# Performance work log

Measured on AMD Instinct MI355X. Metric: run time of the kernel, lower is better.

Reference implementation:

```python
import jax, jax.numpy as jnp
import numpy as np
import itertools

SEQ, NF, K, SD, NB, NC, NOBJ = 8, 4, 3, 256, 512, 174, 10
BELTA, SUB, BATCH = 0.1, 10, 256
SCALES = list(range(NF, 0, -1))  # [4, 3, 2, 1]
D = (K + 1) * SD                 # per-frame fused feature dim = 1024


def _adjust_scales(seq_ind, is_test):
    # mirrors adjust_scale_train / adjust_scale_test
    scale_max = NF * 2
    if seq_ind < scale_max:
        return SCALES[-seq_ind:] if is_test else SCALES[-min(SUB, seq_ind):]
    return SCALES[:min(SUB, seq_ind) + 1]


def _plan(is_test):
    # Static (non-traced) relation-index plan: for each seq_ind, the set of
    # arithmetic-progression frame combinations selected by select_idx().
    plan = []
    for seq_ind in range(1, SEQ + 1):
        entries = []
        for scale in _adjust_scales(seq_ind, is_test):
            k = min(scale, seq_ind)
            division = seq_ind // scale
            sel = [r for r in itertools.combinations(range(seq_ind), k)
                   if np.all(np.diff(np.asarray(r)) == division)]
            if sel:
                entries.append((scale, np.asarray(sel, dtype=np.int32)))
        plan.append(entries)
    return plan


def _temporal_variation(init_input):
    # VLAD-style soft residuals. Source runs kmeans (non-deterministic,
    # numpy/detached); we use deterministic centers = first K points per clip
    # and reproduce the exact downstream math, including the (buggy but
    # faithful) scalar spectral-norm soft assignment shared by all points.
    x = init_input.reshape(-1, SEQ, NOBJ, SD)              # (B, S, O, d)
    flat = x.reshape(x.shape[0], SEQ * NOBJ, SD)           # (B, N, d)
    centers = flat[:, :K, :]                               # (B, K, d)
    diff = flat[:, None, :, :] - centers[:, :, None, :]    # (B, K, N, d)
    sig = jnp.linalg.svd(diff, compute_uv=False)[..., 0]   # matrix 2-norm per (b, k)
    w = jax.nn.softmax(-BELTA * sig ** 2, axis=-1)         # (B, K), same for every point
    # S[b,t,k,:] = sum_o w[b,k] * (x[b,t,o,:] - c[b,k,:])
    var = w[:, None, :, None] * (x.sum(axis=2)[:, :, None, :] - NOBJ * centers[:, None, :, :])
    return jax.lax.stop_gradient(var)  # source detaches via .detach().numpy()


def _fusion(x, w1, b1, w2, b2):
    # Sequential(ReLU, Linear, ReLU, Linear)
    h = jnp.maximum(jax.nn.relu(x) @ w1 + b1, 0.0)
    return h @ w2 + b2


def _forward(graph_out, init_input, params, is_test):
    B = graph_out.shape[0]
    var = _temporal_variation(init_input)                      # (B, S, K, d)
    new_input = jnp.concatenate([var.reshape(B, SEQ, K * SD), graph_out], axis=2)  # (B, S, D)
    rows = []
    for entries in _plan(bool(is_test)):
        acc = jnp.zeros((B, NC), graph_out.dtype)
        for scale, rel in entries:
            # batched gather of all sampled relations at once: (B, R, scale, D)
            g = new_input[:, rel, :].reshape(B, rel.shape[0], scale * D)
            acc = acc + _fusion(g, *params[scale]).sum(axis=1)
        rows.append(acc)
    return jnp.stack(rows, axis=1).reshape(B * SEQ, NC)


def setup_inputs():
    key = jax.random.key(0)
    ks = jax.random.split(key, 2 + 2 * len(SCALES))
    inp = {
        "graph_out": jax.random.normal(ks[0], (BATCH, SEQ, SD), jnp.float32),
        "init_input": jax.random.normal(ks[1], (BATCH * SEQ, NOBJ, SD), jnp.float32),
        "is_test": 0,
    }
    for i, s in enumerate(SCALES):
        inp[f"w1_{s}"] = jax.random.normal(ks[2 + 2 * i], (s * D, NB), jnp.float32) * 0.02
        inp[f"b1_{s}"] = jnp.zeros((NB,), jnp.float32)
        inp[f"w2_{s}"] = jax.random.normal(ks[3 + 2 * i], (NB, NC), jnp.float32) * 0.02
        inp[f"b2_{s}"] = jnp.zeros((NC,), jnp.float32)
    return inp


def reference(graph_out, init_input, is_test, w1_4, b1_4, w2_4, b2_4, w1_3, b1_3, w2_3, b2_3, w1_2, b1_2, w2_2, b2_2, w1_1, b1_1, w2_1, b2_1):
    params = {4: (w1_4, b1_4, w2_4, b2_4), 3: (w1_3, b1_3, w2_3, b2_3),
              2: (w1_2, b1_2, w2_2, b2_2), 1: (w1_1, b1_1, w2_1, b2_1)}
    return _forward(graph_out, init_input, params, is_test)
```

## Files before the change

### kernel.cpp

```cpp
#include <hip/hip_runtime.h>
#include <math.h>
#include <stdint.h>


typedef __attribute__((ext_vector_type(8))) short short8v;
typedef __attribute__((ext_vector_type(4))) short short4v;
typedef __attribute__((ext_vector_type(4))) float f32x4;

__device__ __forceinline__ short f2bf(float f) {
  uint32_t u = __float_as_uint(f);
  u += 0x7fffu + ((u >> 16) & 1u);
  return (short)(u >> 16);
}
__device__ __forceinline__ float bf2f(short s) {
  return __uint_as_float(((uint32_t)(uint16_t)s) << 16);
}
__device__ __forceinline__ void gload16(const void* g, void* l) {
  __builtin_amdgcn_global_load_lds(
      (const __attribute__((address_space(1))) void*)g,
      (__attribute__((address_space(3))) void*)l, 16, 0, 0);
}

__device__ const int8_t ROWS4[12][5] = {
  {3, 0,1,2,3},
  {4, 0,1,2,3},{4, 1,2,3,4},
  {5, 0,1,2,3},{5, 1,2,3,4},{5, 2,3,4,5},
  {6, 0,1,2,3},{6, 1,2,3,4},{6, 2,3,4,5},{6, 3,4,5,6},
  {7, 0,2,4,6},{7, 1,3,5,7},
};
__device__ const int8_t ROWS3[15][4] = {
  {2, 0,1,2},
  {3, 0,1,2},{3, 1,2,3},
  {4, 0,1,2},{4, 1,2,3},{4, 2,3,4},
  {5, 0,2,4},{5, 1,3,5},
  {6, 0,2,4},{6, 1,3,5},{6, 2,4,6},
  {7, 0,2,4},{7, 1,3,5},{7, 2,4,6},{7, 3,5,7},
};
__device__ const int8_t ROWS2[19][3] = {
  {1, 0,1},
  {2, 0,1},{2, 1,2},
  {3, 0,2},{3, 1,3},
  {4, 0,2},{4, 1,3},{4, 2,4},
  {5, 0,3},{5, 1,4},{5, 2,5},
  {6, 0,3},{6, 1,4},{6, 2,5},{6, 3,6},
  {7, 0,4},{7, 1,5},{7, 2,6},{7, 3,7},
};
__device__ const int8_t ROWS1[36][2] = {
  {0,0},
  {1,0},{1,1},
  {2,0},{2,1},{2,2},
  {3,0},{3,1},{3,2},{3,3},
  {4,0},{4,1},{4,2},{4,3},{4,4},
  {5,0},{5,1},{5,2},{5,3},{5,4},{5,5},
  {6,0},{6,1},{6,2},{6,3},{6,4},{6,5},{6,6},
  {7,0},{7,1},{7,2},{7,3},{7,4},{7,5},{7,6},{7,7},
};
__device__ const float CNT[8][4] = {
  {0,0,0,1},{0,0,1,2},{0,1,2,3},{1,2,2,4},
  {2,3,3,5},{3,2,3,6},{4,3,4,7},{2,4,4,8},
};

#define GV_FH    0
#define GV_FL    20480
#define GV_S     40960
#define GV_XSUM  67840
#define GV_VB    76032
#define GV_UU    78048
#define GV_SCAL  79008
#define GV_SZ    79056

__global__ __launch_bounds__(256) void gram_var(
    const float* __restrict__ init, const float* __restrict__ graph,
    short* __restrict__ Rbuf)
{
  __shared__ __align__(16) char smem[GV_SZ];
  short* Fh  = (short*)(smem + GV_FH);
  short* Fl  = (short*)(smem + GV_FL);
  float* Sm  = (float*)(smem + GV_S);
  float* xsm = (float*)(smem + GV_XSUM);
  float* vb  = (float*)(smem + GV_VB);
  float* uum = (float*)(smem + GV_UU);
  float* scal= (float*)(smem + GV_SCAL);

  const int tid = threadIdx.x, lane = tid & 63, w = tid >> 6;
  const int b = blockIdx.x;
  const float* fb = init + (size_t)b * 80 * 256;

  int ti_[7], tj_[7];
#pragma unroll
  for (int q = 0; q < 7; ++q) {
    int tt = w + q * 4;
    int t5 = (tt < 25) ? tt : 0;
    ti_[q] = t5 / 5; tj_[q] = t5 % 5;
  }

  f32x4 acc[7];
#pragma unroll
  for (int q = 0; q < 7; ++q) acc[q] = (f32x4){0.f, 0.f, 0.f, 0.f};

  for (int ch = 0; ch < 2; ++ch) {
    __syncthreads();
    {
      const int t = tid >> 5, kq = tid & 31;
      const float* src = fb + (size_t)(t * 10) * 256 + ch * 128 + kq * 4;
      f32x4 sum = (f32x4){0.f, 0.f, 0.f, 0.f};
#pragma unroll
      for (int o = 0; o < 10; ++o) {
        f32x4 v = *(const f32x4*)(src + (size_t)o * 256);
        int r = t * 10 + o;
        int byte8 = r * 256 + ((kq * 8) ^ ((r & 7) << 4));
        short4v hv, lv;
#pragma unroll
        for (int e = 0; e < 4; ++e) {
          short h = f2bf(v[e]);
          hv[e] = h;
          lv[e] = f2bf(v[e] - bf2f(h));
        }
        *(short4v*)((char*)Fh + byte8) = hv;
        *(short4v*)((char*)Fl + byte8) = lv;
        sum += v;
      }
      *(f32x4*)(xsm + t * 256 + ch * 128 + kq * 4) = sum;
    }
    __syncthreads();

#pragma unroll
    for (int ks = 0; ks < 4; ++ks) {
      const int koff2 = (ks * 32 + (lane >> 4) * 8) * 2;
#pragma unroll
      for (int q = 0; q < 7; ++q) {
        const int tt = w + q * 4;
        if (tt < 25) {
          int ra = ti_[q] * 16 + (lane & 15);
          int rb = tj_[q] * 16 + (lane & 15);
          int ba = ra * 256 + (koff2 ^ ((ra & 7) << 4));
          int bb = rb * 256 + (koff2 ^ ((rb & 7) << 4));
          short8v ah = *(const short8v*)((char*)Fh + ba);
          short8v al = *(const short8v*)((char*)Fl + ba);
          short8v bh = *(const short8v*)((char*)Fh + bb);
          short8v bl = *(const short8v*)((char*)Fl + bb);
          acc[q] = __builtin_amdgcn_mfma_f32_16x16x32_bf16(ah, bh, acc[q], 0, 0, 0);
          acc[q] = __builtin_amdgcn_mfma_f32_16x16x32_bf16(ah, bl, acc[q], 0, 0, 0);
          acc[q] = __builtin_amdgcn_mfma_f32_16x16x32_bf16(al, bh, acc[q], 0, 0, 0);
        }
      }
    }
  }

#pragma unroll
  for (int q = 0; q < 7; ++q) {
    const int tt = w + q * 4;
    if (tt < 25) {
      int row0 = ti_[q] * 16 + (lane >> 4) * 4;
      int col = tj_[q] * 16 + (lane & 15);
#pragma unroll
      for (int r = 0; r < 4; ++r) Sm[(row0 + r) * 84 + col] = acc[q][r];
    }
  }
  if (tid < 240) vb[(0 * 3 + tid / 80) * 84 + (tid % 80)] = 1.0f;
  __syncthreads();

  const int pk = (tid < 240) ? tid / 80 : 0;
  const int pi = (tid < 240) ? tid % 80 : 0;
  int cur = 0;
  for (int it = 0; it < 5; ++it) {
    const bool last = (it == 4);
    float u = 0.f;
    if (tid < 240) {
      const float* Si = Sm + pi * 84;
      const float* vk = vb + (cur * 3 + pk) * 84;
#pragma unroll
      for (int q2 = 0; q2 < 20; ++q2) {
        f32x4 aa = *(const f32x4*)(Si + q2 * 4);
        f32x4 vv = *(const f32x4*)(vk + q2 * 4);
        u += aa.x * vv.x + aa.y * vv.y + aa.z * vv.z + aa.w * vv.w;
      }
    } else if (tid < 246) {
      int w2 = tid - 240;
      int k = (w2 < 3) ? w2 : w2 - 3;
      const float* vk = vb + (cur * 3 + k) * 84;
      float s = 0.f;
      if (w2 < 3) {
        for (int j2 = 0; j2 < 80; ++j2) s += vk[j2];
        scal[k] = s;
      } else {
        const float* Sk = Sm + k * 84;
        for (int j2 = 0; j2 < 80; ++j2) s += Sk[j2] * vk[j2];
        scal[3 + k] = s;
      }
    }
    __syncthreads();
    if (tid < 240) {
      float sg = scal[pk], tu = scal[3 + pk];
      float un = u - Sm[pi * 84 + pk] * sg - tu + Sm[pk * 84 + pk] * sg;
      if (!last) vb[((cur ^ 1) * 3 + pk) * 84 + pi] = un * 6.103515625e-05f;
      else       uum[pk * 80 + pi] = un;
    }
    __syncthreads();
    if (!last) cur ^= 1;
  }

  if (tid < 192) {
    const int k = tid >> 6, ln = tid & 63;
    float v1 = vb[(cur * 3 + k) * 84 + ln];
    float u1 = uum[k * 80 + ln];
    float a = u1 * v1, b2 = v1 * v1;
    if (ln < 16) {
      float v2 = vb[(cur * 3 + k) * 84 + 64 + ln];
      float u2 = uum[k * 80 + 64 + ln];
      a += u2 * v2; b2 += v2 * v2;
    }
#pragma unroll
    for (int m = 32; m >= 1; m >>= 1) {
      a += __shfl_xor(a, m);
      b2 += __shfl_xor(b2, m);
    }
    if (ln == 0) scal[9 + k] = a / b2;
  }
  __syncthreads();
  if (tid == 0) {
    float L0 = -0.1f * scal[9], L1 = -0.1f * scal[10], L2 = -0.1f * scal[11];
    float m = fmaxf(L0, fmaxf(L1, L2));
    float e0 = expf(L0 - m), e1 = expf(L1 - m), e2 = expf(L2 - m);
    float inv = 1.0f / (e0 + e1 + e2);
    scal[6] = e0 * inv; scal[7] = e1 * inv; scal[8] = e2 * inv;
  }
  __syncthreads();

  {
    const float w0 = scal[6], w1 = scal[7], w2 = scal[8];
    const int d0 = (tid & 63) * 4;
#pragma unroll
    for (int p = 0; p < 2; ++p) {
      const int t = p * 4 + (tid >> 6);
      f32x4 xs = *(const f32x4*)(xsm + t * 256 + d0);
      f32x4 c0 = *(const f32x4*)(fb + 0 * 256 + d0);
      f32x4 c1 = *(const f32x4*)(fb + 1 * 256 + d0);
      f32x4 c2 = *(const f32x4*)(fb + 2 * 256 + d0);
      f32x4 go = *(const f32x4*)(graph + (size_t)(b * 8 + t) * 256 + d0);
      size_t rb = ((size_t)(b * 8 + t)) * 1024;
      short4v s0, s1, s2, s3;
#pragma unroll
      for (int q = 0; q < 4; ++q) {
        float xq = xs[q];
        s0[q] = f2bf(fmaxf(w0 * (xq - 10.f * c0[q]), 0.f));
        s1[q] = f2bf(fmaxf(w1 * (xq - 10.f * c1[q]), 0.f));
        s2[q] = f2bf(fmaxf(w2 * (xq - 10.f * c2[q]), 0.f));
        s3[q] = f2bf(fmaxf(go[q], 0.f));
      }
      *(short4v*)&Rbuf[rb + 0 + d0]   = s0;
      *(short4v*)&Rbuf[rb + 256 + d0] = s1;
      *(short4v*)&Rbuf[rb + 512 + d0] = s2;
      *(short4v*)&Rbuf[rb + 768 + d0] = s3;
    }
  }
}

__global__ __launch_bounds__(512) void prep_weights(
    const float* __restrict__ w1_4, const float* __restrict__ w1_3,
    const float* __restrict__ w1_2, const float* __restrict__ w1_1,
    const float* __restrict__ w2a, const float* __restrict__ w2b,
    const float* __restrict__ w2c, const float* __restrict__ w2d,
    short* __restrict__ W1T, short* __restrict__ W2T)
{
  __shared__ float sh[64 * 65];
  const int blk = blockIdx.x, tid = threadIdx.x;
  if (blk < 1280) {
    const int slice = blk >> 7, rem = blk & 127;
    const int k0 = (rem & 15) * 64, c0 = (rem >> 4) * 64;
    const float* W1; int j;
    if (slice < 4)      { W1 = w1_4; j = slice; }
    else if (slice < 7) { W1 = w1_3; j = slice - 4; }
    else if (slice < 9) { W1 = w1_2; j = slice - 7; }
    else                { W1 = w1_1; j = 0; }
#pragma unroll
    for (int q = tid; q < 1024; q += 512) {
      int r = q >> 4, cq = (q & 15) * 4;
      f32x4 v = *(const f32x4*)(W1 + (size_t)(j * 1024 + k0 + r) * 512 + c0 + cq);
      sh[r * 65 + cq + 0] = v.x; sh[r * 65 + cq + 1] = v.y;
      sh[r * 65 + cq + 2] = v.z; sh[r * 65 + cq + 3] = v.w;
    }
    __syncthreads();
#pragma unroll
    for (int q = tid; q < 1024; q += 512) {
      int cc = q >> 4, kq = (q & 15) * 4;
      short4v sv;
#pragma unroll
      for (int m = 0; m < 4; ++m) sv[m] = f2bf(sh[(kq + m) * 65 + cc]);
      *(short4v*)&W1T[(size_t)(slice * 512 + c0 + cc) * 1024 + k0 + kq] = sv;
    }
  } else {
    int idx = (blk - 1280) * 2048 + tid * 4;
    int col = idx >> 11, kg = idx & 2047;
    int si = kg >> 9, kr = kg & 511;
    const float* w = (si == 0) ? w2a : (si == 1) ? w2b : (si == 2) ? w2c : w2d;
    short4v sv;
#pragma unroll
    for (int q = 0; q < 4; ++q)
      sv[q] = (col < 174) ? f2bf(w[(size_t)(kr + q) * 174 + col]) : (short)0;
    *(short4v*)&W2T[idx] = sv;
  }
}

__global__ __launch_bounds__(256) void p_mfma(
    const short* __restrict__ A, const short* __restrict__ W1T,
    short* __restrict__ P)
{
  __shared__ short As[128 * 32];
  __shared__ short Bs[128 * 32];
  const int id = blockIdx.x + blockIdx.y * 40;
  const int nid = (id & 7) * 80 + (id >> 3);
  const int bx = nid >> 4, by = nid & 15;
  const int tid = threadIdx.x, lane = tid & 63, w = tid >> 6;
  const int wr = w >> 1, wc = w & 1;
  const int rowBase = by * 128;
  const short* Bp = W1T + (size_t)bx * 128 * 1024;
  const int rA = w * 16 + (lane >> 2);
  const int kkA = (lane & 3) * 8;

  f32x4 acc[4][4];
#pragma unroll
  for (int m = 0; m < 4; ++m)
#pragma unroll
    for (int n = 0; n < 4; ++n) acc[m][n] = (f32x4){0.f, 0.f, 0.f, 0.f};

  for (int k0 = 0; k0 < 1024; k0 += 32) {
    __syncthreads();
    gload16(A + (size_t)(rowBase + rA) * 1024 + k0 + kkA, As + w * 512);
    gload16(A + (size_t)(rowBase + 64 + rA) * 1024 + k0 + kkA, As + 2048 + w * 512);
    gload16(Bp + (size_t)rA * 1024 + k0 + kkA, Bs + w * 512);
    gload16(Bp + (size_t)(64 + rA) * 1024 + k0 + kkA, Bs + 2048 + w * 512);
    __syncthreads();
    short8v a[4], bv[4];
#pragma unroll
    for (int m = 0; m < 4; ++m)
      a[m] = *(const short8v*)(As + (wr * 64 + m * 16 + (lane & 15)) * 32 + (lane >> 4) * 8);
#pragma unroll
    for (int n = 0; n < 4; ++n)
      bv[n] = *(const short8v*)(Bs + (wc * 64 + n * 16 + (lane & 15)) * 32 + (lane >> 4) * 8);
#pragma unroll
    for (int m = 0; m < 4; ++m)
#pragma unroll
      for (int n = 0; n < 4; ++n)
        acc[m][n] = __builtin_amdgcn_mfma_f32_16x16x32_bf16(a[m], bv[n], acc[m][n], 0, 0, 0);
  }

  const int colG = bx * 128 + wc * 64;
#pragma unroll
  for (int m = 0; m < 4; ++m) {
    int row = rowBase + wr * 64 + m * 16 + (lane >> 4) * 4;
#pragma unroll
    for (int n = 0; n < 4; ++n) {
      int col = colG + n * 16 + (lane & 15);
#pragma unroll
      for (int r = 0; r < 4; ++r)
        P[(size_t)(row + r) * 5120 + col] = f2bf(acc[m][n][r]);
    }
  }
}

__global__ __launch_bounds__(256) void hsum_all(
    const short* __restrict__ P,
    const float* __restrict__ b1a, const float* __restrict__ b1b,
    const float* __restrict__ b1c, const float* __restrict__ b1d,
    short* __restrict__ Hsum)
{
  const int row = blockIdx.x, t = row & 7, base = row - t;
  const int c0 = threadIdx.x * 2;
  const size_t prow = (size_t)base * 5120;

  {
    float2 bb = *(const float2*)(b1a + c0);
    float a0 = 0.f, a1 = 0.f;
    for (int r = 0; r < 12; ++r) {
      if (ROWS4[r][0] != t) continue;
      float h0 = bb.x, h1 = bb.y;
#pragma unroll
      for (int jj = 0; jj < 4; ++jj) {
        const short2 pv = *(const short2*)(P + prow + (size_t)ROWS4[r][1 + jj] * 5120 + jj * 512 + c0);
        h0 += bf2f(pv.x); h1 += bf2f(pv.y);
      }
      a0 += fmaxf(h0, 0.f); a1 += fmaxf(h1, 0.f);
    }
    uint32_t wv = (uint32_t)(uint16_t)f2bf(a0) | ((uint32_t)(uint16_t)f2bf(a1) << 16);
    *(uint32_t*)&Hsum[(size_t)row * 2048 + c0] = wv;
  }
  {
    float2 bb = *(const float2*)(b1b + c0);
    float a0 = 0.f, a1 = 0.f;
    for (int r = 0; r < 15; ++r) {
      if (ROWS3[r][0] != t) continue;
      float h0 = bb.x, h1 = bb.y;
#pragma unroll
      for (int jj = 0; jj < 3; ++jj) {
        const short2 pv = *(const short2*)(P + prow + (size_t)ROWS3[r][1 + jj] * 5120 + 2048 + jj * 512 + c0);
        h0 += bf2f(pv.x); h1 += bf2f(pv.y);
      }
      a0 += fmaxf(h0, 0.f); a1 += fmaxf(h1, 0.f);
    }
    uint32_t wv = (uint32_t)(uint16_t)f2bf(a0) | ((uint32_t)(uint16_t)f2bf(a1) << 16);
    *(uint32_t*)&Hsum[(size_t)row * 2048 + 512 + c0] = wv;
  }
  {
    float2 bb = *(const float2*)(b1c + c0);
    float a0 = 0.f, a1 = 0.f;
    for (int r = 0; r < 19; ++r) {
      if (ROWS2[r][0] != t) continue;
      float h0 = bb.x, h1 = bb.y;
#pragma unroll
      for (int jj = 0; jj < 2; ++jj) {
        const short2 pv = *(const short2*)(P + prow + (size_t)ROWS2[r][1 + jj] * 5120 + 3584 + jj * 512 + c0);
        h0 += bf2f(pv.x); h1 += bf2f(pv.y);
      }
      a0 += fmaxf(h0, 0.f); a1 += fmaxf(h1, 0.f);
    }
    uint32_t wv = (uint32_t)(uint16_t)f2bf(a0) | ((uint32_t)(uint16_t)f2bf(a1) << 16);
    *(uint32_t*)&Hsum[(size_t)row * 2048 + 1024 + c0] = wv;
  }
  {
    float2 bb = *(const float2*)(b1d + c0);
    float a0 = 0.f, a1 = 0.f;
    for (int r = 0; r < 36; ++r) {
      if (ROWS1[r][0] != t) continue;
      const short2 pv = *(const short2*)(P + prow + (size_t)ROWS1[r][1] * 5120 + 4608 + c0);
      a0 += fmaxf(bb.x + bf2f(pv.x), 0.f);
      a1 += fmaxf(bb.y + bf2f(pv.y), 0.f);
    }
    uint32_t wv = (uint32_t)(uint16_t)f2bf(a0) | ((uint32_t)(uint16_t)f2bf(a1) << 16);
    *(uint32_t*)&Hsum[(size_t)row * 2048 + 1536 + c0] = wv;
  }
}

__global__ __launch_bounds__(256) void out_split(
    const short* __restrict__ H, const short* __restrict__ W2T,
    float* __restrict__ partial)
{
  __shared__ short As[128 * 32];
  __shared__ short Bs[64 * 32];
  const int tid = threadIdx.x, lane = tid & 63, w = tid >> 6;
  const int wr = w >> 1, wc = w & 1;
  const int rowBase = blockIdx.y * 128, colBase = blockIdx.x * 64;
  const int kBase = blockIdx.z * 512;
  const int rA = w * 16 + (lane >> 2);
  const int kkA = (lane & 3) * 8;

  f32x4 acc[4][2];
#pragma unroll
  for (int m = 0; m < 4; ++m)
#pragma unroll
    for (int n = 0; n < 2; ++n) acc[m][n] = (f32x4){0.f, 0.f, 0.f, 0.f};

  for (int k0 = 0; k0 < 512; k0 += 32) {
    const int kg = kBase + k0;
    __syncthreads();
    gload16(H + (size_t)(rowBase + rA) * 2048 + kg + kkA, As + w * 512);
    gload16(H + (size_t)(rowBase + 64 + rA) * 2048 + kg + kkA, As + 2048 + w * 512);
    gload16(W2T + (size_t)(colBase + rA) * 2048 + kg + kkA, Bs + w * 512);
    __syncthreads();
    short8v a[4], bv[2];
#pragma unroll
    for (int m = 0; m < 4; ++m)
      a[m] = *(const short8v*)(As + (wr * 64 + m * 16 + (lane & 15)) * 32 + (lane >> 4) * 8);
#pragma unroll
    for (int n = 0; n < 2; ++n)
      bv[n] = *(const short8v*)(Bs + (wc * 32 + n * 16 + (lane & 15)) * 32 + (lane >> 4) * 8);
#pragma unroll
    for (int m = 0; m < 4; ++m)
#pragma unroll
      for (int n = 0; n < 2; ++n)
        acc[m][n] = __builtin_amdgcn_mfma_f32_16x16x32_bf16(a[m], bv[n], acc[m][n], 0, 0, 0);
  }

  float* pz = partial + (size_t)blockIdx.z * 2048 * 192;
#pragma unroll
  for (int n = 0; n < 2; ++n) {
    int col = colBase + wc * 32 + n * 16 + (lane & 15);
#pragma unroll
    for (int m = 0; m < 4; ++m) {
      int row0 = rowBase + wr * 64 + m * 16 + (lane >> 4) * 4;
#pragma unroll
      for (int r = 0; r < 4; ++r)
        pz[(size_t)(row0 + r) * 192 + col] = acc[m][n][r];
    }
  }
}

__global__ __launch_bounds__(256) void out_reduce(
    const float* __restrict__ partial,
    const float* __restrict__ b2a, const float* __restrict__ b2b,
    const float* __restrict__ b2c, const float* __restrict__ b2d,
    float* __restrict__ out)
{
  const int row = blockIdx.x, col = threadIdx.x;
  if (col >= 174) return;
  const size_t o = (size_t)row * 192 + col;
  float s = partial[o] + partial[o + (size_t)2048 * 192]
          + partial[o + (size_t)4096 * 192] + partial[o + (size_t)6144 * 192];
  int tt = row & 7;
  float bias = CNT[tt][0] * b2a[col] + CNT[tt][1] * b2b[col]
             + CNT[tt][2] * b2c[col] + CNT[tt][3] * b2d[col];
  out[(size_t)row * 174 + col] = s + bias;
}

extern "C" void kernel_launch(void* const* d_in, const int* in_sizes, int n_in,
                              void* d_out, int out_size, void* d_ws, size_t ws_size,
                              hipStream_t stream) {
  const float* graph = (const float*)d_in[0];
  const float* init  = (const float*)d_in[1];
  const float* w1[4] = {(const float*)d_in[3],  (const float*)d_in[7],
                        (const float*)d_in[11], (const float*)d_in[15]};
  const float* b1[4] = {(const float*)d_in[4],  (const float*)d_in[8],
                        (const float*)d_in[12], (const float*)d_in[16]};
  const float* w2[4] = {(const float*)d_in[5],  (const float*)d_in[9],
                        (const float*)d_in[13], (const float*)d_in[17]};
  const float* b2[4] = {(const float*)d_in[6],  (const float*)d_in[10],
                        (const float*)d_in[14], (const float*)d_in[18]};
  float* out = (float*)d_out;

  char* ws = (char*)d_ws;
  short* Rbf  = (short*)(ws + 0);
  short* W1T  = (short*)(ws + ((size_t)4  << 20));
  short* P    = (short*)(ws + ((size_t)14 << 20));
  short* W2T  = (short*)(ws + ((size_t)34 << 20));
  short* Hsum = (short*)(ws + 0);
  float* Part = (float*)(ws + ((size_t)8 << 20));

  gram_var<<<256, 256, 0, stream>>>(init, graph, Rbf);

  prep_weights<<<1472, 512, 0, stream>>>(w1[0], w1[1], w1[2], w1[3],
                                         w2[0], w2[1], w2[2], w2[3], W1T, W2T);

  p_mfma<<<dim3(40, 16), 256, 0, stream>>>(Rbf, W1T, P);

  hsum_all<<<2048, 256, 0, stream>>>(P, b1[0], b1[1], b1[2], b1[3], Hsum);

  out_split<<<dim3(3, 16, 4), 256, 0, stream>>>(Hsum, W2T, Part);

  out_reduce<<<2048, 256, 0, stream>>>(Part, b2[0], b2[1], b2[2], b2[3], out);
}
```

Baseline: 94.45 us.

## Compute only needed frame-slot projections in P GEMM and vectorize hsum

The projection GEMM previously computed all 10 weight-slice columns for every frame row, although each slice is only consumed for a contiguous subset of frame positions. It now enumerates (slice, row-tile, col-tile) work items and gathers only the frame rows each slice actually uses, storing P in a compact per-slice layout. The GEMM blocks drop from 640 to 408, with matching reductions in P write traffic. hsum_all is updated to index the compact layout and now processes two rows per block with 4-wide vector loads. This adds per-row div/mod index math and a gathered A-load pattern.

```diff
diff --git a/kernel.cpp b/kernel.cpp
--- a/kernel.cpp
+++ b/kernel.cpp
@@ -60,6 +60,11 @@
   {2,3,3,5},{3,2,3,6},{4,3,4,7},{2,4,4,8},
 };
 
+__device__ const int SL_LO[10]  = {0,1,2,3, 0,1,2, 0,1, 0};
+__device__ const int SL_LEN[10] = {4,4,4,5, 4,5,6, 4,7, 8};
+__device__ const int SL_PB[10]  = {0,4,8,12,17,21,26,32,36,43};
+__device__ const int SL_MT[10]  = {0,8,16,24,34,42,52,64,72,86};
+
 #define GV_FH    0
 #define GV_FL    20480
 #define GV_S     40960
@@ -308,15 +313,26 @@
 {
   __shared__ short As[128 * 32];
   __shared__ short Bs[128 * 32];
-  const int id = blockIdx.x + blockIdx.y * 40;
-  const int nid = (id & 7) * 80 + (id >> 3);
-  const int bx = nid >> 4, by = nid & 15;
+  const int id = blockIdx.x;
+  const int nid = (id & 7) * 51 + (id >> 3);
+  const int ctile = nid & 3;
+  const int rest = nid >> 2;
+  int sl = 0;
+#pragma unroll
+  for (int q = 1; q < 10; ++q) if (rest >= SL_MT[q]) sl = q;
+  const int mt = rest - SL_MT[sl];
+  const int lo = SL_LO[sl];
+  const unsigned len = (unsigned)SL_LEN[sl];
+  short* Pp = P + (size_t)SL_PB[sl] * 131072;
+  const short* Bp = W1T + ((size_t)sl * 512 + (size_t)ctile * 128) * 1024;
+
   const int tid = threadIdx.x, lane = tid & 63, w = tid >> 6;
   const int wr = w >> 1, wc = w & 1;
-  const int rowBase = by * 128;
-  const short* Bp = W1T + (size_t)bx * 128 * 1024;
   const int rA = w * 16 + (lane >> 2);
   const int kkA = (lane & 3) * 8;
+  const unsigned lr0 = (unsigned)(mt * 128 + rA), lr1 = lr0 + 64u;
+  const int gr0 = (int)((lr0 / len) * 8u + lo + (lr0 % len));
+  const int gr1 = (int)((lr1 / len) * 8u + lo + (lr1 % len));
 
   f32x4 acc[4][4];
 #pragma unroll
@@ -326,8 +342,8 @@
 
   for (int k0 = 0; k0 < 1024; k0 += 32) {
     __syncthreads();
-    gload16(A + (size_t)(rowBase + rA) * 1024 + k0 + kkA, As + w * 512);
-    gload16(A + (size_t)(rowBase + 64 + rA) * 1024 + k0 + kkA, As + 2048 + w * 512);
+    gload16(A + (size_t)gr0 * 1024 + k0 + kkA, As + w * 512);
+    gload16(A + (size_t)gr1 * 1024 + k0 + kkA, As + 2048 + w * 512);
     gload16(Bp + (size_t)rA * 1024 + k0 + kkA, Bs + w * 512);
     gload16(Bp + (size_t)(64 + rA) * 1024 + k0 + kkA, Bs + 2048 + w * 512);
     __syncthreads();
@@ -345,16 +361,15 @@
         acc[m][n] = __builtin_amdgcn_mfma_f32_16x16x32_bf16(a[m], bv[n], acc[m][n], 0, 0, 0);
   }
 
-  const int colG = bx * 128 + wc * 64;
 #pragma unroll
   for (int m = 0; m < 4; ++m) {
-    int row = rowBase + wr * 64 + m * 16 + (lane >> 4) * 4;
+    int lrow = mt * 128 + wr * 64 + m * 16 + (lane >> 4) * 4;
 #pragma unroll
     for (int n = 0; n < 4; ++n) {
-      int col = colG + n * 16 + (lane & 15);
+      int col = ctile * 128 + wc * 64 + n * 16 + (lane & 15);
 #pragma unroll
       for (int r = 0; r < 4; ++r)
-        P[(size_t)(row + r) * 5120 + col] = f2bf(acc[m][n][r]);
+        Pp[(size_t)(lrow + r) * 512 + col] = f2bf(acc[m][n][r]);
     }
   }
 }
@@ -365,69 +380,98 @@
     const float* __restrict__ b1c, const float* __restrict__ b1d,
     short* __restrict__ Hsum)
 {
-  const int row = blockIdx.x, t = row & 7, base = row - t;
-  const int c0 = threadIdx.x * 2;
-  const size_t prow = (size_t)base * 5120;
+  const int tid = threadIdx.x;
+  const int row = blockIdx.x * 2 + (tid >> 7);
+  const int t = row & 7;
+  const size_t bq = (size_t)(row >> 3);
+  const int c0 = (tid & 127) * 4;
 
   {
-    float2 bb = *(const float2*)(b1a + c0);
-    float a0 = 0.f, a1 = 0.f;
+    const int pb[4] = {0, 4 * 131072, 8 * 131072, 12 * 131072};
+    const int lo[4] = {0, 1, 2, 3};
+    const int ln[4] = {4, 4, 4, 5};
+    f32x4 bb = *(const f32x4*)(b1a + c0);
+    f32x4 a = (f32x4){0.f, 0.f, 0.f, 0.f};
     for (int r = 0; r < 12; ++r) {
       if (ROWS4[r][0] != t) continue;
-      float h0 = bb.x, h1 = bb.y;
+      f32x4 h = bb;
 #pragma unroll
       for (int jj = 0; jj < 4; ++jj) {
-        const short2 pv = *(const short2*)(P + prow + (size_t)ROWS4[r][1 + jj] * 5120 + jj * 512 + c0);
-        h0 += bf2f(pv.x); h1 += bf2f(pv.y);
-      }
-      a0 += fmaxf(h0, 0.f); a1 += fmaxf(h1, 0.f);
-    }
-    uint32_t wv = (uint32_t)(uint16_t)f2bf(a0) | ((uint32_t)(uint16_t)f2bf(a1) << 16);
-    *(uint32_t*)&Hsum[(size_t)row * 2048 + c0] = wv;
+        const short4v pv = *(const short4v*)(P + pb[jj] +
+            (bq * ln[jj] + (ROWS4[r][1 + jj] - lo[jj])) * 512 + c0);
+#pragma unroll
+        for (int e = 0; e < 4; ++e) h[e] += bf2f(pv[e]);
+      }
+#pragma unroll
+      for (int e = 0; e < 4; ++e) a[e] += fmaxf(h[e], 0.f);
+    }
+    short4v sv;
+#pragma unroll
+    for (int e = 0; e < 4; ++e) sv[e] = f2bf(a[e]);
+    *(short4v*)&Hsum[(size_t)row * 2048 + c0] = sv;
   }
   {
-    float2 bb = *(const float2*)(b1b + c0);
-    float a0 = 0.f, a1 = 0.f;
+    const int pb[3] = {17 * 131072, 21 * 131072, 26 * 131072};
+    const int lo[3] = {0, 1, 2};
+    const int ln[3] = {4, 5, 6};
+    f32x4 bb = *(const f32x4*)(b1b + c0);
+    f32x4 a = (f32x4){0.f, 0.f, 0.f, 0.f};
     for (int r = 0; r < 15; ++r) {
       if (ROWS3[r][0] != t) continue;
-      float h0 = bb.x, h1 = bb.y;
+      f32x4 h = bb;
 #pragma unroll
       for (int jj = 0; jj < 3; ++jj) {
-        const short2 pv = *(const short2*)(P + prow + (size_t)ROWS3[r][1 + jj] * 5120 + 2048 + jj * 512 + c0);
-        h0 += bf2f(pv.x); h1 += bf2f(pv.y);
-      }
-      a0 += fmaxf(h0, 0.f); a1 += fmaxf(h1, 0.f);
-    }
-    uint32_t wv = (uint32_t)(uint16_t)f2bf(a0) | ((uint32_t)(uint16_t)f2bf(a1) << 16);
-    *(uint32_t*)&Hsum[(size_t)row * 2048 + 512 + c0] = wv;
+        const short4v pv = *(const short4v*)(P + pb[jj] +
+            (bq * ln[jj] + (ROWS3[r][1 + jj] - lo[jj])) * 512 + c0);
+#pragma unroll
+        for (int e = 0; e < 4; ++e) h[e] += bf2f(pv[e]);
+      }
+#pragma unroll
+      for (int e = 0; e < 4; ++e) a[e] += fmaxf(h[e], 0.f);
+    }
+    short4v sv;
+#pragma unroll
+    for (int e = 0; e < 4; ++e) sv[e] = f2bf(a[e]);
+    *(short4v*)&Hsum[(size_t)row * 2048 + 512 + c0] = sv;
   }
   {
-    float2 bb = *(const float2*)(b1c + c0);
-    float a0 = 0.f, a1 = 0.f;
+    const int pb[2] = {32 * 131072, 36 * 131072};
+    const int lo[2] = {0, 1};
+    const int ln[2] = {4, 7};
+    f32x4 bb = *(const f32x4*)(b1c + c0);
+    f32x4 a = (f32x4){0.f, 0.f, 0.f, 0.f};
     for (int r = 0; r < 19; ++r) {
       if (ROWS2[r][0] != t) continue;
-      float h0 = bb.x, h1 = bb.y;
+      f32x4 h = bb;
 #pragma unroll
       for (int jj = 0; jj < 2; ++jj) {
-        const short2 pv = *(const short2*)(P + prow + (size_t)ROWS2[r][1 + jj] * 5120 + 3584 + jj * 512 + c0);
-        h0 += bf2f(pv.x); h1 += bf2f(pv.y);
-      }
-      a0 += fmaxf(h0, 0.f); a1 += fmaxf(h1, 0.f);
-    }
-    uint32_t wv = (uint32_t)(uint16_t)f2bf(a0) | ((uint32_t)(uint16_t)f2bf(a1) << 16);
-    *(uint32_t*)&Hsum[(size_t)row * 2048 + 1024 + c0] = wv;
+        const short4v pv = *(const short4v*)(P + pb[jj] +
+            (bq * ln[jj] + (ROWS2[r][1 + jj] - lo[jj])) * 512 + c0);
+#pragma unroll
+        for (int e = 0; e < 4; ++e) h[e] += bf2f(pv[e]);
+      }
+#pragma unroll
+      for (int e = 0; e < 4; ++e) a[e] += fmaxf(h[e], 0.f);
+    }
+    short4v sv;
+#pragma unroll
+    for (int e = 0; e < 4; ++e) sv[e] = f2bf(a[e]);
+    *(short4v*)&Hsum[(size_t)row * 2048 + 1024 + c0] = sv;
   }
   {
-    float2 bb = *(const float2*)(b1d + c0);
-    float a0 = 0.f, a1 = 0.f;
+    f32x4 bb = *(const f32x4*)(b1d + c0);
+    f32x4 a = (f32x4){0.f, 0.f, 0.f, 0.f};
     for (int r = 0; r < 36; ++r) {
       if (ROWS1[r][0] != t) continue;
-      const short2 pv = *(const short2*)(P + prow + (size_t)ROWS1[r][1] * 5120 + 4608 + c0);
-      a0 += fmaxf(bb.x + bf2f(pv.x), 0.f);
-      a1 += fmaxf(bb.y + bf2f(pv.y), 0.f);
-    }
-    uint32_t wv = (uint32_t)(uint16_t)f2bf(a0) | ((uint32_t)(uint16_t)f2bf(a1) << 16);
-    *(uint32_t*)&Hsum[(size_t)row * 2048 + 1536 + c0] = wv;
+      const short4v pv = *(const short4v*)(P + 43 * 131072 +
+          (bq * 8 + ROWS1[r][1]) * 512 + c0);
+#pragma unroll
+      for (int e = 0; e < 4; ++e) a[e] += fmaxf(bb[e] + bf2f(pv[e]), 0.f);
+    }
+    short4v sv;
+#pragma unroll
+    for (int e = 0; e < 4; ++e) sv[e] = f2bf(a[e]);
+    *(short4v*)&Hsum[(size_t)row * 2048 + 1536 + c0] = sv;
   }
 }
 
@@ -530,9 +574,9 @@
   prep_weights<<<1472, 512, 0, stream>>>(w1[0], w1[1], w1[2], w1[3],
                                          w2[0], w2[1], w2[2], w2[3], W1T, W2T);
 
-  p_mfma<<<dim3(40, 16), 256, 0, stream>>>(Rbf, W1T, P);
-
-  hsum_all<<<2048, 256, 0, stream>>>(P, b1[0], b1[1], b1[2], b1[3], Hsum);
+  p_mfma<<<408, 256, 0, stream>>>(Rbf, W1T, P);
+
+  hsum_all<<<1024, 256, 0, stream>>>(P, b1[0], b1[1], b1[2], b1[3], Hsum);
 
   out_split<<<dim3(3, 16, 4), 256, 0, stream>>>(Hsum, W2T, Part);
 
```

New measurement: 98.14 us. 3.9% more time.
